# Performance work log

Measured on AMD Instinct MI355X. Metric: run time of the kernel, lower is better.

Reference implementation:

```python
import jax, jax.numpy as jnp
import numpy as np
import math

B, S, D, H = 4, 1024, 1024, 16

def setup_inputs() -> dict:
    key = jax.random.key(0)
    ks = jax.random.split(key, 9)
    Q = jax.random.normal(ks[0], (B, S, D), dtype=jnp.float32)
    K = jax.random.normal(ks[1], (B, S, D), dtype=jnp.float32)
    V = jax.random.normal(ks[2], (B, S, D), dtype=jnp.float32)
    mask = jax.random.randint(ks[3], (B, 1, S, S), 0, 2, dtype=jnp.int32)
    # keep the diagonal unmasked so no causal row is fully -inf (avoids NaN softmax rows)
    eye = jnp.eye(S, dtype=jnp.int32)[None, None]
    mask = jnp.maximum(mask, eye)
    sc = 1.0 / math.sqrt(D)
    Wq = jax.random.normal(ks[4], (D, D), dtype=jnp.float32) * sc
    Wk = jax.random.normal(ks[5], (D, D), dtype=jnp.float32) * sc
    Wv = jax.random.normal(ks[6], (D, D), dtype=jnp.float32) * sc
    Wo = jax.random.normal(ks[7], (D, D), dtype=jnp.float32) * sc
    bo = jnp.zeros((D,), dtype=jnp.float32)
    return {"Q": Q, "K": K, "V": V, "mask": mask,
            "Wq": Wq, "Wk": Wk, "Wv": Wv, "Wo": Wo, "bo": bo, "heads": H}


def reference(Q, K, V, mask, Wq, Wk, Wv, Wo, bo, heads):
    b, s, d = Q.shape
    dk = d // heads
    # QKV projections (bias-free) and head split: [B,S,D] -> [B,H,S,dk]
    def split_heads(x, W):
        return (x @ W).reshape(b, s, heads, dk).transpose(0, 2, 1, 3)
    q = split_heads(Q, Wq)
    k = split_heads(K, Wk)
    v = split_heads(V, Wv)
    # raw scores [B,H,S,S]
    attn = jnp.einsum('bhqd,bhkd->bhqk', q, k) / jnp.sqrt(jnp.float32(dk))
    # multiplicative padding mask
    attn = attn * mask.astype(attn.dtype)
    # sequential=True: torch.tril zeroes the strict upper triangle
    causal = jnp.tril(jnp.ones((s, s), dtype=attn.dtype))
    attn = attn * causal
    # the module's quirk: exact zeros become -inf before softmax
    attn = jnp.where(attn == 0, -jnp.inf, attn)
    scores = jax.nn.softmax(attn, axis=-1)  # dropout is identity in eval / p=0
    ctx = jnp.einsum('bhqk,bhkd->bhqd', scores, v)
    concat = ctx.transpose(0, 2, 1, 3).reshape(b, s, d)
    return concat @ Wo + bo
```

## Files before the change

### kernel.cpp

```cpp
#include <hip/hip_runtime.h>

#define DEV __device__ __forceinline__

typedef __bf16 bf16x8 __attribute__((ext_vector_type(8)));
typedef float f32x4 __attribute__((ext_vector_type(4)));
typedef unsigned short u16x4 __attribute__((ext_vector_type(4)));
typedef unsigned short u16x8 __attribute__((ext_vector_type(8)));
typedef unsigned int u32;

DEV unsigned short f2bf(float f) {
  union { float f; unsigned int u; } v; v.f = f;
  unsigned int r = v.u + 0x7fffu + ((v.u >> 16) & 1u);
  return (unsigned short)(r >> 16);
}

DEV int swz(int row, int kbyte) { return row * 128 + (kbyte ^ ((row & 7) << 4)); }

__global__ __launch_bounds__(256) void pack_mask_k(const int* __restrict__ mask,
                                                   u32* __restrict__ bits) {
  int e = blockIdx.x * 256 + threadIdx.x;
  int m = mask[e];
  unsigned long long b = __ballot(m != 0);
  int lane = threadIdx.x & 63;
  if (lane == 0)       bits[e >> 5] = (u32)b;
  else if (lane == 32) bits[e >> 5] = (u32)(b >> 32);
}

__global__ __launch_bounds__(256) void wtrans_k(
    const float* __restrict__ W0, const float* __restrict__ W1,
    const float* __restrict__ W2, const float* __restrict__ W3,
    unsigned short* __restrict__ O0, unsigned short* __restrict__ O1,
    unsigned short* __restrict__ O2, unsigned short* __restrict__ O3) {
  const float* W = blockIdx.z == 0 ? W0 : blockIdx.z == 1 ? W1 : blockIdx.z == 2 ? W2 : W3;
  unsigned short* O = blockIdx.z == 0 ? O0 : blockIdx.z == 1 ? O1 : blockIdx.z == 2 ? O2 : O3;
  __shared__ float tile[32][33];
  int tx = threadIdx.x, ty = threadIdx.y;
  int x0 = blockIdx.x * 32, y0 = blockIdx.y * 32;
  #pragma unroll
  for (int i = 0; i < 4; i++)
    tile[ty + i * 8][tx] = W[(size_t)(y0 + ty + i * 8) * 1024 + x0 + tx];
  __syncthreads();
  #pragma unroll
  for (int i = 0; i < 4; i++)
    O[(size_t)(x0 + ty + i * 8) * 1024 + y0 + tx] = f2bf(tile[tx][ty + i * 8]);
}

__global__ __launch_bounds__(256) void proj_gemm_k(
    const float* __restrict__ Qx, const float* __restrict__ Kx, const float* __restrict__ Vx,
    const unsigned short* __restrict__ Wtq, const unsigned short* __restrict__ Wtk,
    const unsigned short* __restrict__ Wtv,
    unsigned short* __restrict__ qo, unsigned short* __restrict__ ko,
    unsigned short* __restrict__ vo) {
  int z = blockIdx.z;
  const float* X = z == 0 ? Qx : z == 1 ? Kx : Vx;
  const unsigned short* Wt = z == 0 ? Wtq : z == 1 ? Wtk : Wtv;
  unsigned short* out = z == 0 ? qo : z == 1 ? ko : vo;

  __shared__ __align__(16) unsigned short As[128 * 64];
  __shared__ __align__(16) unsigned short Bs[128 * 64];

  int t = threadIdx.x;
  int m0 = blockIdx.x * 128, n0 = blockIdx.y * 128;
  int w = t >> 6, lane = t & 63;
  int wm = (w >> 1) * 64, wn = (w & 1) * 64;
  int rl = lane & 15, kgrp = lane >> 4;

  f32x4 acc[4][4];
  #pragma unroll
  for (int m = 0; m < 4; m++)
    #pragma unroll
    for (int n = 0; n < 4; n++)
      #pragma unroll
      for (int r = 0; r < 4; r++) acc[m][n][r] = 0.f;

  for (int kt = 0; kt < 16; kt++) {
    __syncthreads();
    #pragma unroll
    for (int i = 0; i < 8; i++) {
      int e = (i * 256 + t) * 4;
      int r = e >> 6, c = e & 63;
      f32x4 xv = *(const f32x4*)(X + (size_t)(m0 + r) * 1024 + kt * 64 + c);
      u16x4 p;
      p[0] = f2bf(xv[0]); p[1] = f2bf(xv[1]); p[2] = f2bf(xv[2]); p[3] = f2bf(xv[3]);
      *(u16x4*)((char*)As + swz(r, c * 2)) = p;
    }
    #pragma unroll
    for (int i = 0; i < 4; i++) {
      int e = (i * 256 + t) * 8;
      int r = e >> 6, c = e & 63;
      u16x8 bv = *(const u16x8*)(Wt + (size_t)(n0 + r) * 1024 + kt * 64 + c);
      *(u16x8*)((char*)Bs + swz(r, c * 2)) = bv;
    }
    __syncthreads();
    #pragma unroll
    for (int kk = 0; kk < 2; kk++) {
      bf16x8 af[4], bfr[4];
      #pragma unroll
      for (int m = 0; m < 4; m++)
        af[m] = *(const bf16x8*)((const char*)As + swz(wm + m * 16 + rl, kk * 64 + kgrp * 16));
      #pragma unroll
      for (int n = 0; n < 4; n++)
        bfr[n] = *(const bf16x8*)((const char*)Bs + swz(wn + n * 16 + rl, kk * 64 + kgrp * 16));
      #pragma unroll
      for (int m = 0; m < 4; m++)
        #pragma unroll
        for (int n = 0; n < 4; n++)
          acc[m][n] = __builtin_amdgcn_mfma_f32_16x16x32_bf16(af[m], bfr[n], acc[m][n], 0, 0, 0);
    }
  }
  #pragma unroll
  for (int m = 0; m < 4; m++)
    #pragma unroll
    for (int n = 0; n < 4; n++)
      #pragma unroll
      for (int r = 0; r < 4; r++) {
        int grow = m0 + wm + m * 16 + kgrp * 4 + r;
        int gcol = n0 + wn + n * 16 + rl;
        int b = grow >> 10, s = grow & 1023;
        int h = gcol >> 6, d = gcol & 63;
        if (z == 2)
          out[(size_t)((b * 16 + h) * 64 + d) * 1024 + s] = f2bf(acc[m][n][r]);
        else
          out[(size_t)((b * 16 + h) * 1024 + s) * 64 + d] = f2bf(acc[m][n][r]);
      }
}

__global__ __launch_bounds__(256) void attn_k(
    const unsigned short* __restrict__ qg, const unsigned short* __restrict__ kg,
    const unsigned short* __restrict__ vtg, const u32* __restrict__ mbits,
    unsigned short* __restrict__ concat) {
  int p = blockIdx.x;
  int bh = blockIdx.y;
  int b = bh >> 4, h = bh & 15;
  int t = threadIdx.x, w = t >> 6, lane = t & 63;
  int rl = lane & 15, kgrp = lane >> 4;

  const int qtA = p, qtB = 15 - p, J = qtB + 1;
  const int q0s[2] = {qtA * 64, qtB * 64};

  __shared__ __align__(16) unsigned short Ks[2][64 * 64];
  __shared__ __align__(16) unsigned short Vt[2][64 * 64];
  __shared__ __align__(16) unsigned short Ps[4][16 * 64];

  const size_t headoff = (size_t)bh * 65536;

  bf16x8 qa[2][2];
  #pragma unroll
  for (int tl = 0; tl < 2; tl++) {
    int row = q0s[tl] + w * 16 + rl;
    #pragma unroll
    for (int kk = 0; kk < 2; kk++)
      qa[tl][kk] = *(const bf16x8*)(qg + headoff + (size_t)row * 64 + kk * 32 + kgrp * 8);
  }

  u16x8 kst[2], vst[2];
  #pragma unroll
  for (int i = 0; i < 2; i++) {
    int e = (i * 256 + t) * 8, r = e >> 6, c = e & 63;
    kst[i] = *(const u16x8*)(kg  + headoff + (size_t)r * 64 + c);
    vst[i] = *(const u16x8*)(vtg + headoff + (size_t)r * 1024 + c);
  }

  float mrow[2][4], lrow[2][4];
  f32x4 acc[2][4];
  #pragma unroll
  for (int tl = 0; tl < 2; tl++)
    #pragma unroll
    for (int r = 0; r < 4; r++) {
      mrow[tl][r] = -1e30f; lrow[tl][r] = 0.f;
      #pragma unroll
      for (int d = 0; d < 4; d++) acc[tl][d][r] = 0.f;
    }

  for (int j = 0; j < J; j++) {
    unsigned short* Kb = (unsigned short*)Ks[j & 1];
    unsigned short* Vb = (unsigned short*)Vt[j & 1];
    #pragma unroll
    for (int i = 0; i < 2; i++) {
      int e = (i * 256 + t) * 8, r = e >> 6, c = e & 63;
      *(u16x8*)((char*)Kb + swz(r, c * 2)) = kst[i];
      *(u16x8*)((char*)Vb + swz(r, c * 2)) = vst[i];
    }
    __syncthreads();
    if (j + 1 < J) {
      #pragma unroll
      for (int i = 0; i < 2; i++) {
        int e = (i * 256 + t) * 8, r = e >> 6, c = e & 63;
        kst[i] = *(const u16x8*)(kg  + headoff + (size_t)((j + 1) * 64 + r) * 64 + c);
        vst[i] = *(const u16x8*)(vtg + headoff + (size_t)r * 1024 + (j + 1) * 64 + c);
      }
    }

    #pragma unroll
    for (int tl = 1; tl >= 0; tl--) {
      if (tl == 0 && j > qtA) continue;
      const int q0 = q0s[tl];
      f32x4 sc[4];
      #pragma unroll
      for (int n = 0; n < 4; n++) {
        f32x4 z4;
        #pragma unroll
        for (int r = 0; r < 4; r++) z4[r] = 0.f;
        bf16x8 kb0 = *(const bf16x8*)((const char*)Kb + swz(n * 16 + rl, 0 * 64 + kgrp * 16));
        bf16x8 kb1 = *(const bf16x8*)((const char*)Kb + swz(n * 16 + rl, 1 * 64 + kgrp * 16));
        z4 = __builtin_amdgcn_mfma_f32_16x16x32_bf16(qa[tl][0], kb0, z4, 0, 0, 0);
        sc[n] = __builtin_amdgcn_mfma_f32_16x16x32_bf16(qa[tl][1], kb1, z4, 0, 0, 0);
      }
      int qrow[4]; u32 w0[4], w1[4];
      #pragma unroll
      for (int r = 0; r < 4; r++) {
        qrow[r] = q0 + w * 16 + kgrp * 4 + r;
        size_t base = ((size_t)b * 1024 + qrow[r]) * 32 + j * 2;
        w0[r] = mbits[base]; w1[r] = mbits[base + 1];
      }
      float pv[4][4];
      #pragma unroll
      for (int n = 0; n < 4; n++) {
        int kvloc = n * 16 + rl;
        int kvg = j * 64 + kvloc;
        #pragma unroll
        for (int r = 0; r < 4; r++) {
          u32 wsel = (n < 2) ? w0[r] : w1[r];
          int bit = (wsel >> (kvloc & 31)) & 1;
          float val = sc[n][r] * 0.125f;
          bool keep = bit && (kvg <= qrow[r]) && (val != 0.f);
          pv[n][r] = keep ? val : -1e30f;
        }
      }
      #pragma unroll
      for (int r = 0; r < 4; r++) {
        float vmax = fmaxf(fmaxf(pv[0][r], pv[1][r]), fmaxf(pv[2][r], pv[3][r]));
        vmax = fmaxf(vmax, __shfl_xor(vmax, 1));
        vmax = fmaxf(vmax, __shfl_xor(vmax, 2));
        vmax = fmaxf(vmax, __shfl_xor(vmax, 4));
        vmax = fmaxf(vmax, __shfl_xor(vmax, 8));
        float mnew = fmaxf(mrow[tl][r], vmax);
        float alpha = __expf(mrow[tl][r] - mnew);
        mrow[tl][r] = mnew;
        float ts = 0.f;
        #pragma unroll
        for (int n = 0; n < 4; n++) {
          float pe = __expf(pv[n][r] - mnew);
          pv[n][r] = pe;
          ts += pe;
        }
        ts += __shfl_xor(ts, 1); ts += __shfl_xor(ts, 2);
        ts += __shfl_xor(ts, 4); ts += __shfl_xor(ts, 8);
        lrow[tl][r] = lrow[tl][r] * alpha + ts;
        #pragma unroll
        for (int d = 0; d < 4; d++) acc[tl][d][r] *= alpha;
      }
      unsigned short* pb = &Ps[w][0];
      #pragma unroll
      for (int n = 0; n < 4; n++) {
        int col = n * 16 + rl;
        #pragma unroll
        for (int r = 0; r < 4; r++)
          *(unsigned short*)((char*)pb + swz(kgrp * 4 + r, col * 2)) = f2bf(pv[n][r]);
      }
      bf16x8 pa[2];
      #pragma unroll
      for (int kk = 0; kk < 2; kk++)
        pa[kk] = *(const bf16x8*)((const char*)pb + swz(rl, kk * 64 + kgrp * 16));
      #pragma unroll
      for (int d = 0; d < 4; d++) {
        bf16x8 vb0 = *(const bf16x8*)((const char*)Vb + swz(d * 16 + rl, 0 * 64 + kgrp * 16));
        bf16x8 vb1 = *(const bf16x8*)((const char*)Vb + swz(d * 16 + rl, 1 * 64 + kgrp * 16));
        acc[tl][d] = __builtin_amdgcn_mfma_f32_16x16x32_bf16(pa[0], vb0, acc[tl][d], 0, 0, 0);
        acc[tl][d] = __builtin_amdgcn_mfma_f32_16x16x32_bf16(pa[1], vb1, acc[tl][d], 0, 0, 0);
      }
    }
  }
  #pragma unroll
  for (int tl = 0; tl < 2; tl++)
    #pragma unroll
    for (int r = 0; r < 4; r++) {
      float linv = 1.f / lrow[tl][r];
      int srow = q0s[tl] + w * 16 + kgrp * 4 + r;
      size_t rowoff = ((size_t)b * 1024 + srow) * 1024 + h * 64;
      #pragma unroll
      for (int d = 0; d < 4; d++)
        concat[rowoff + d * 16 + rl] = f2bf(acc[tl][d][r] * linv);
    }
}

__global__ __launch_bounds__(256) void out_gemm_k(
    const unsigned short* __restrict__ A, const unsigned short* __restrict__ Wt,
    const float* __restrict__ bias, float* __restrict__ out) {
  __shared__ __align__(16) unsigned short As[128 * 64];
  __shared__ __align__(16) unsigned short Bs[128 * 64];

  int t = threadIdx.x;
  int m0 = blockIdx.x * 128, n0 = blockIdx.y * 128;
  int w = t >> 6, lane = t & 63;
  int wm = (w >> 1) * 64, wn = (w & 1) * 64;
  int rl = lane & 15, kgrp = lane >> 4;

  f32x4 acc[4][4];
  #pragma unroll
  for (int m = 0; m < 4; m++)
    #pragma unroll
    for (int n = 0; n < 4; n++)
      #pragma unroll
      for (int r = 0; r < 4; r++) acc[m][n][r] = 0.f;

  for (int kt = 0; kt < 16; kt++) {
    __syncthreads();
    #pragma unroll
    for (int i = 0; i < 4; i++) {
      int e = (i * 256 + t) * 8;
      int r = e >> 6, c = e & 63;
      u16x8 av = *(const u16x8*)(A + (size_t)(m0 + r) * 1024 + kt * 64 + c);
      *(u16x8*)((char*)As + swz(r, c * 2)) = av;
    }
    #pragma unroll
    for (int i = 0; i < 4; i++) {
      int e = (i * 256 + t) * 8;
      int r = e >> 6, c = e & 63;
      u16x8 bv = *(const u16x8*)(Wt + (size_t)(n0 + r) * 1024 + kt * 64 + c);
      *(u16x8*)((char*)Bs + swz(r, c * 2)) = bv;
    }
    __syncthreads();
    #pragma unroll
    for (int kk = 0; kk < 2; kk++) {
      bf16x8 af[4], bfr[4];
      #pragma unroll
      for (int m = 0; m < 4; m++)
        af[m] = *(const bf16x8*)((const char*)As + swz(wm + m * 16 + rl, kk * 64 + kgrp * 16));
      #pragma unroll
      for (int n = 0; n < 4; n++)
        bfr[n] = *(const bf16x8*)((const char*)Bs + swz(wn + n * 16 + rl, kk * 64 + kgrp * 16));
      #pragma unroll
      for (int m = 0; m < 4; m++)
        #pragma unroll
        for (int n = 0; n < 4; n++)
          acc[m][n] = __builtin_amdgcn_mfma_f32_16x16x32_bf16(af[m], bfr[n], acc[m][n], 0, 0, 0);
    }
  }
  #pragma unroll
  for (int m = 0; m < 4; m++)
    #pragma unroll
    for (int n = 0; n < 4; n++)
      #pragma unroll
      for (int r = 0; r < 4; r++) {
        int grow = m0 + wm + m * 16 + kgrp * 4 + r;
        int gcol = n0 + wn + n * 16 + rl;
        out[(size_t)grow * 1024 + gcol] = acc[m][n][r] + bias[gcol];
      }
}

extern "C" void kernel_launch(void* const* d_in, const int* in_sizes, int n_in,
                              void* d_out, int out_size, void* d_ws, size_t ws_size,
                              hipStream_t stream) {
  const float* Q  = (const float*)d_in[0];
  const float* K  = (const float*)d_in[1];
  const float* V  = (const float*)d_in[2];
  const int* mask = (const int*)d_in[3];
  const float* Wq = (const float*)d_in[4];
  const float* Wk = (const float*)d_in[5];
  const float* Wv = (const float*)d_in[6];
  const float* Wo = (const float*)d_in[7];
  const float* bo = (const float*)d_in[8];
  float* out = (float*)d_out;

  char* ws = (char*)d_ws;
  unsigned short* qb  = (unsigned short*)(ws);
  unsigned short* kb  = (unsigned short*)(ws + (8u  << 20));
  unsigned short* vb  = (unsigned short*)(ws + (16u << 20));
  unsigned short* cc  = (unsigned short*)(ws + (24u << 20));
  unsigned short* wqt = (unsigned short*)(ws + (32u << 20));
  unsigned short* wkt = (unsigned short*)(ws + (34u << 20));
  unsigned short* wvt = (unsigned short*)(ws + (36u << 20));
  unsigned short* wot = (unsigned short*)(ws + (38u << 20));
  u32*            mb  = (u32*)(ws + (40u << 20));

  pack_mask_k<<<16384, 256, 0, stream>>>(mask, mb);
  wtrans_k<<<dim3(32, 32, 4), dim3(32, 8), 0, stream>>>(Wq, Wk, Wv, Wo, wqt, wkt, wvt, wot);
  proj_gemm_k<<<dim3(32, 8, 3), 256, 0, stream>>>(Q, K, V, wqt, wkt, wvt, qb, kb, vb);
  attn_k<<<dim3(8, 64), 256, 0, stream>>>(qb, kb, vb, mb, cc);
  out_gemm_k<<<dim3(32, 8), 256, 0, stream>>>(cc, wot, bo, out);
}
```

Baseline: 264.5 us.

## Pre-pack operands into swizzled tiles and load via global_load_lds

Adds a separate kernel that converts Q/K/V to bf16 and stores them pre-tiled in the swizzled LDS layout. The transposed weights, the K/V projection outputs and the attention output are written in the same tile-packed layout. This lets the GEMMs and the attention kernel copy tiles straight from global memory into LDS with global_load_lds, bypassing registers and the per-element swizzle arithmetic. The cost is an extra cast kernel pass over the fp32 inputs and scattered 2-byte stores in the epilogues. The GEMM main loops stay single-buffered.

```diff
diff --git a/kernel.cpp b/kernel.cpp
--- a/kernel.cpp
+++ b/kernel.cpp
@@ -4,7 +4,6 @@
 
 typedef __bf16 bf16x8 __attribute__((ext_vector_type(8)));
 typedef float f32x4 __attribute__((ext_vector_type(4)));
-typedef unsigned short u16x4 __attribute__((ext_vector_type(4)));
 typedef unsigned short u16x8 __attribute__((ext_vector_type(8)));
 typedef unsigned int u32;
 
@@ -15,6 +14,12 @@
 }
 
 DEV int swz(int row, int kbyte) { return row * 128 + (kbyte ^ ((row & 7) << 4)); }
+
+DEV void gload16(const void* g, void* l) {
+  __builtin_amdgcn_global_load_lds(
+      (const __attribute__((address_space(1))) unsigned int*)g,
+      (__attribute__((address_space(3))) unsigned int*)l, 16, 0, 0);
+}
 
 __global__ __launch_bounds__(256) void pack_mask_k(const int* __restrict__ mask,
                                                    u32* __restrict__ bits) {
@@ -24,6 +29,32 @@
   int lane = threadIdx.x & 63;
   if (lane == 0)       bits[e >> 5] = (u32)b;
   else if (lane == 32) bits[e >> 5] = (u32)(b >> 32);
+}
+
+__global__ __launch_bounds__(256) void xcast_k(
+    const float* __restrict__ Qx, const float* __restrict__ Kx, const float* __restrict__ Vx,
+    unsigned short* __restrict__ qp, unsigned short* __restrict__ kp,
+    unsigned short* __restrict__ vp) {
+  int z = blockIdx.y;
+  const float* X = z == 0 ? Qx : z == 1 ? Kx : Vx;
+  unsigned short* P = z == 0 ? qp : z == 1 ? kp : vp;
+  int tile = blockIdx.x;
+  int mb = tile >> 4, kt = tile & 15;
+  int t = threadIdx.x;
+  size_t tb = (size_t)tile * 16384;
+  #pragma unroll
+  for (int i = 0; i < 4; i++) {
+    int idx = i * 256 + t;
+    int r = idx >> 3, j = idx & 7;
+    int c0 = ((j * 16) ^ ((r & 7) << 4)) >> 1;
+    const float* src = X + (size_t)(mb * 128 + r) * 1024 + kt * 64 + c0;
+    f32x4 a = *(const f32x4*)src;
+    f32x4 bq = *(const f32x4*)(src + 4);
+    u16x8 o;
+    o[0] = f2bf(a[0]); o[1] = f2bf(a[1]); o[2] = f2bf(a[2]); o[3] = f2bf(a[3]);
+    o[4] = f2bf(bq[0]); o[5] = f2bf(bq[1]); o[6] = f2bf(bq[2]); o[7] = f2bf(bq[3]);
+    *(u16x8*)((char*)P + tb + (size_t)idx * 16) = o;
+  }
 }
 
 __global__ __launch_bounds__(256) void wtrans_k(
@@ -41,27 +72,29 @@
     tile[ty + i * 8][tx] = W[(size_t)(y0 + ty + i * 8) * 1024 + x0 + tx];
   __syncthreads();
   #pragma unroll
-  for (int i = 0; i < 4; i++)
-    O[(size_t)(x0 + ty + i * 8) * 1024 + y0 + tx] = f2bf(tile[tx][ty + i * 8]);
+  for (int i = 0; i < 4; i++) {
+    int n = x0 + ty + i * 8, k = y0 + tx;
+    size_t a = (size_t)((n >> 7) * 16 + (k >> 6)) * 16384 + swz(n & 127, (k & 63) * 2);
+    *(unsigned short*)((char*)O + a) = f2bf(tile[tx][ty + i * 8]);
+  }
 }
 
 __global__ __launch_bounds__(256) void proj_gemm_k(
-    const float* __restrict__ Qx, const float* __restrict__ Kx, const float* __restrict__ Vx,
+    const unsigned short* __restrict__ Qp, const unsigned short* __restrict__ Kp,
+    const unsigned short* __restrict__ Vp,
     const unsigned short* __restrict__ Wtq, const unsigned short* __restrict__ Wtk,
     const unsigned short* __restrict__ Wtv,
     unsigned short* __restrict__ qo, unsigned short* __restrict__ ko,
     unsigned short* __restrict__ vo) {
   int z = blockIdx.z;
-  const float* X = z == 0 ? Qx : z == 1 ? Kx : Vx;
-  const unsigned short* Wt = z == 0 ? Wtq : z == 1 ? Wtk : Wtv;
+  const unsigned short* Ap = z == 0 ? Qp : z == 1 ? Kp : Vp;
+  const unsigned short* Bp = z == 0 ? Wtq : z == 1 ? Wtk : Wtv;
   unsigned short* out = z == 0 ? qo : z == 1 ? ko : vo;
 
-  __shared__ __align__(16) unsigned short As[128 * 64];
-  __shared__ __align__(16) unsigned short Bs[128 * 64];
-
-  int t = threadIdx.x;
-  int m0 = blockIdx.x * 128, n0 = blockIdx.y * 128;
-  int w = t >> 6, lane = t & 63;
+  __shared__ __align__(16) unsigned short As[8192];
+  __shared__ __align__(16) unsigned short Bs[8192];
+
+  int t = threadIdx.x, w = t >> 6, lane = t & 63;
   int wm = (w >> 1) * 64, wn = (w & 1) * 64;
   int rl = lane & 15, kgrp = lane >> 4;
 
@@ -75,21 +108,14 @@
 
   for (int kt = 0; kt < 16; kt++) {
     __syncthreads();
-    #pragma unroll
-    for (int i = 0; i < 8; i++) {
-      int e = (i * 256 + t) * 4;
-      int r = e >> 6, c = e & 63;
-      f32x4 xv = *(const f32x4*)(X + (size_t)(m0 + r) * 1024 + kt * 64 + c);
-      u16x4 p;
-      p[0] = f2bf(xv[0]); p[1] = f2bf(xv[1]); p[2] = f2bf(xv[2]); p[3] = f2bf(xv[3]);
-      *(u16x4*)((char*)As + swz(r, c * 2)) = p;
-    }
+    const char* ab = (const char*)Ap + (size_t)(blockIdx.x * 16 + kt) * 16384 + w * 1024 + lane * 16;
+    const char* bb = (const char*)Bp + (size_t)(blockIdx.y * 16 + kt) * 16384 + w * 1024 + lane * 16;
+    char* al = (char*)As + w * 1024;
+    char* bl = (char*)Bs + w * 1024;
     #pragma unroll
     for (int i = 0; i < 4; i++) {
-      int e = (i * 256 + t) * 8;
-      int r = e >> 6, c = e & 63;
-      u16x8 bv = *(const u16x8*)(Wt + (size_t)(n0 + r) * 1024 + kt * 64 + c);
-      *(u16x8*)((char*)Bs + swz(r, c * 2)) = bv;
+      gload16(ab + i * 4096, al + i * 4096);
+      gload16(bb + i * 4096, bl + i * 4096);
     }
     __syncthreads();
     #pragma unroll
@@ -108,6 +134,7 @@
           acc[m][n] = __builtin_amdgcn_mfma_f32_16x16x32_bf16(af[m], bfr[n], acc[m][n], 0, 0, 0);
     }
   }
+  int m0 = blockIdx.x * 128, n0 = blockIdx.y * 128;
   #pragma unroll
   for (int m = 0; m < 4; m++)
     #pragma unroll
@@ -118,17 +145,23 @@
         int gcol = n0 + wn + n * 16 + rl;
         int b = grow >> 10, s = grow & 1023;
         int h = gcol >> 6, d = gcol & 63;
-        if (z == 2)
-          out[(size_t)((b * 16 + h) * 64 + d) * 1024 + s] = f2bf(acc[m][n][r]);
-        else
-          out[(size_t)((b * 16 + h) * 1024 + s) * 64 + d] = f2bf(acc[m][n][r]);
+        unsigned short val = f2bf(acc[m][n][r]);
+        if (z == 0) {
+          out[(size_t)((b * 16 + h) * 1024 + s) * 64 + d] = val;
+        } else if (z == 1) {
+          *(unsigned short*)((char*)out +
+            (size_t)((b * 16 + h) * 16 + (s >> 6)) * 8192 + swz(s & 63, d * 2)) = val;
+        } else {
+          *(unsigned short*)((char*)out +
+            (size_t)((b * 16 + h) * 16 + (s >> 6)) * 8192 + swz(d, (s & 63) * 2)) = val;
+        }
       }
 }
 
 __global__ __launch_bounds__(256) void attn_k(
-    const unsigned short* __restrict__ qg, const unsigned short* __restrict__ kg,
-    const unsigned short* __restrict__ vtg, const u32* __restrict__ mbits,
-    unsigned short* __restrict__ concat) {
+    const unsigned short* __restrict__ qg, const unsigned short* __restrict__ kp,
+    const unsigned short* __restrict__ vp, const u32* __restrict__ mbits,
+    unsigned short* __restrict__ ccp) {
   int p = blockIdx.x;
   int bh = blockIdx.y;
   int b = bh >> 4, h = bh & 15;
@@ -138,11 +171,13 @@
   const int qtA = p, qtB = 15 - p, J = qtB + 1;
   const int q0s[2] = {qtA * 64, qtB * 64};
 
-  __shared__ __align__(16) unsigned short Ks[2][64 * 64];
-  __shared__ __align__(16) unsigned short Vt[2][64 * 64];
-  __shared__ __align__(16) unsigned short Ps[4][16 * 64];
-
-  const size_t headoff = (size_t)bh * 65536;
+  __shared__ __align__(16) unsigned short Ks[2][4096];
+  __shared__ __align__(16) unsigned short Vs[2][4096];
+  __shared__ __align__(16) unsigned short Ps[4][1024];
+
+  const size_t qoff = (size_t)bh * 65536;
+  const char* kbase = (const char*)kp + (size_t)bh * 131072;
+  const char* vbase = (const char*)vp + (size_t)bh * 131072;
 
   bf16x8 qa[2][2];
   #pragma unroll
@@ -150,15 +185,16 @@
     int row = q0s[tl] + w * 16 + rl;
     #pragma unroll
     for (int kk = 0; kk < 2; kk++)
-      qa[tl][kk] = *(const bf16x8*)(qg + headoff + (size_t)row * 64 + kk * 32 + kgrp * 8);
-  }
-
-  u16x8 kst[2], vst[2];
-  #pragma unroll
-  for (int i = 0; i < 2; i++) {
-    int e = (i * 256 + t) * 8, r = e >> 6, c = e & 63;
-    kst[i] = *(const u16x8*)(kg  + headoff + (size_t)r * 64 + c);
-    vst[i] = *(const u16x8*)(vtg + headoff + (size_t)r * 1024 + c);
+      qa[tl][kk] = *(const bf16x8*)(qg + qoff + (size_t)row * 64 + kk * 32 + kgrp * 8);
+  }
+
+  {
+    const char* kg = kbase + w * 1024 + lane * 16;
+    const char* vg = vbase + w * 1024 + lane * 16;
+    char* kl = (char*)Ks[0] + w * 1024;
+    char* vl = (char*)Vs[0] + w * 1024;
+    gload16(kg, kl); gload16(kg + 4096, kl + 4096);
+    gload16(vg, vl); gload16(vg + 4096, vl + 4096);
   }
 
   float mrow[2][4], lrow[2][4];
@@ -173,23 +209,18 @@
     }
 
   for (int j = 0; j < J; j++) {
-    unsigned short* Kb = (unsigned short*)Ks[j & 1];
-    unsigned short* Vb = (unsigned short*)Vt[j & 1];
-    #pragma unroll
-    for (int i = 0; i < 2; i++) {
-      int e = (i * 256 + t) * 8, r = e >> 6, c = e & 63;
-      *(u16x8*)((char*)Kb + swz(r, c * 2)) = kst[i];
-      *(u16x8*)((char*)Vb + swz(r, c * 2)) = vst[i];
-    }
     __syncthreads();
     if (j + 1 < J) {
-      #pragma unroll
-      for (int i = 0; i < 2; i++) {
-        int e = (i * 256 + t) * 8, r = e >> 6, c = e & 63;
-        kst[i] = *(const u16x8*)(kg  + headoff + (size_t)((j + 1) * 64 + r) * 64 + c);
-        vst[i] = *(const u16x8*)(vtg + headoff + (size_t)r * 1024 + (j + 1) * 64 + c);
-      }
-    }
+      int nb = (j + 1) & 1;
+      const char* kg = kbase + (size_t)(j + 1) * 8192 + w * 1024 + lane * 16;
+      const char* vg = vbase + (size_t)(j + 1) * 8192 + w * 1024 + lane * 16;
+      char* kl = (char*)Ks[nb] + w * 1024;
+      char* vl = (char*)Vs[nb] + w * 1024;
+      gload16(kg, kl); gload16(kg + 4096, kl + 4096);
+      gload16(vg, vl); gload16(vg + 4096, vl + 4096);
+    }
+    const char* Kb = (const char*)Ks[j & 1];
+    const char* Vb = (const char*)Vs[j & 1];
 
     #pragma unroll
     for (int tl = 1; tl >= 0; tl--) {
@@ -201,8 +232,8 @@
         f32x4 z4;
         #pragma unroll
         for (int r = 0; r < 4; r++) z4[r] = 0.f;
-        bf16x8 kb0 = *(const bf16x8*)((const char*)Kb + swz(n * 16 + rl, 0 * 64 + kgrp * 16));
-        bf16x8 kb1 = *(const bf16x8*)((const char*)Kb + swz(n * 16 + rl, 1 * 64 + kgrp * 16));
+        bf16x8 kb0 = *(const bf16x8*)(Kb + swz(n * 16 + rl, 0 * 64 + kgrp * 16));
+        bf16x8 kb1 = *(const bf16x8*)(Kb + swz(n * 16 + rl, 1 * 64 + kgrp * 16));
         z4 = __builtin_amdgcn_mfma_f32_16x16x32_bf16(qa[tl][0], kb0, z4, 0, 0, 0);
         sc[n] = __builtin_amdgcn_mfma_f32_16x16x32_bf16(qa[tl][1], kb1, z4, 0, 0, 0);
       }
@@ -264,8 +295,8 @@
         pa[kk] = *(const bf16x8*)((const char*)pb + swz(rl, kk * 64 + kgrp * 16));
       #pragma unroll
       for (int d = 0; d < 4; d++) {
-        bf16x8 vb0 = *(const bf16x8*)((const char*)Vb + swz(d * 16 + rl, 0 * 64 + kgrp * 16));
-        bf16x8 vb1 = *(const bf16x8*)((const char*)Vb + swz(d * 16 + rl, 1 * 64 + kgrp * 16));
+        bf16x8 vb0 = *(const bf16x8*)(Vb + swz(d * 16 + rl, 0 * 64 + kgrp * 16));
+        bf16x8 vb1 = *(const bf16x8*)(Vb + swz(d * 16 + rl, 1 * 64 + kgrp * 16));
         acc[tl][d] = __builtin_amdgcn_mfma_f32_16x16x32_bf16(pa[0], vb0, acc[tl][d], 0, 0, 0);
         acc[tl][d] = __builtin_amdgcn_mfma_f32_16x16x32_bf16(pa[1], vb1, acc[tl][d], 0, 0, 0);
       }
@@ -277,22 +308,22 @@
     for (int r = 0; r < 4; r++) {
       float linv = 1.f / lrow[tl][r];
       int srow = q0s[tl] + w * 16 + kgrp * 4 + r;
-      size_t rowoff = ((size_t)b * 1024 + srow) * 1024 + h * 64;
+      int grow = b * 1024 + srow;
+      char* tbase = (char*)ccp + (size_t)((grow >> 7) * 16 + h) * 16384;
+      int rr = grow & 127;
       #pragma unroll
       for (int d = 0; d < 4; d++)
-        concat[rowoff + d * 16 + rl] = f2bf(acc[tl][d][r] * linv);
+        *(unsigned short*)(tbase + swz(rr, (d * 16 + rl) * 2)) = f2bf(acc[tl][d][r] * linv);
     }
 }
 
 __global__ __launch_bounds__(256) void out_gemm_k(
-    const unsigned short* __restrict__ A, const unsigned short* __restrict__ Wt,
+    const unsigned short* __restrict__ Ap, const unsigned short* __restrict__ Bp,
     const float* __restrict__ bias, float* __restrict__ out) {
-  __shared__ __align__(16) unsigned short As[128 * 64];
-  __shared__ __align__(16) unsigned short Bs[128 * 64];
-
-  int t = threadIdx.x;
-  int m0 = blockIdx.x * 128, n0 = blockIdx.y * 128;
-  int w = t >> 6, lane = t & 63;
+  __shared__ __align__(16) unsigned short As[8192];
+  __shared__ __align__(16) unsigned short Bs[8192];
+
+  int t = threadIdx.x, w = t >> 6, lane = t & 63;
   int wm = (w >> 1) * 64, wn = (w & 1) * 64;
   int rl = lane & 15, kgrp = lane >> 4;
 
@@ -306,19 +337,14 @@
 
   for (int kt = 0; kt < 16; kt++) {
     __syncthreads();
+    const char* ab = (const char*)Ap + (size_t)(blockIdx.x * 16 + kt) * 16384 + w * 1024 + lane * 16;
+    const char* bb = (const char*)Bp + (size_t)(blockIdx.y * 16 + kt) * 16384 + w * 1024 + lane * 16;
+    char* al = (char*)As + w * 1024;
+    char* bl = (char*)Bs + w * 1024;
     #pragma unroll
     for (int i = 0; i < 4; i++) {
-      int e = (i * 256 + t) * 8;
-      int r = e >> 6, c = e & 63;
-      u16x8 av = *(const u16x8*)(A + (size_t)(m0 + r) * 1024 + kt * 64 + c);
-      *(u16x8*)((char*)As + swz(r, c * 2)) = av;
-    }
-    #pragma unroll
-    for (int i = 0; i < 4; i++) {
-      int e = (i * 256 + t) * 8;
-      int r = e >> 6, c = e & 63;
-      u16x8 bv = *(const u16x8*)(Wt + (size_t)(n0 + r) * 1024 + kt * 64 + c);
-      *(u16x8*)((char*)Bs + swz(r, c * 2)) = bv;
+      gload16(ab + i * 4096, al + i * 4096);
+      gload16(bb + i * 4096, bl + i * 4096);
     }
     __syncthreads();
     #pragma unroll
@@ -337,6 +363,7 @@
           acc[m][n] = __builtin_amdgcn_mfma_f32_16x16x32_bf16(af[m], bfr[n], acc[m][n], 0, 0, 0);
     }
   }
+  int m0 = blockIdx.x * 128, n0 = blockIdx.y * 128;
   #pragma unroll
   for (int m = 0; m < 4; m++)
     #pragma unroll
@@ -364,19 +391,23 @@
   float* out = (float*)d_out;
 
   char* ws = (char*)d_ws;
-  unsigned short* qb  = (unsigned short*)(ws);
-  unsigned short* kb  = (unsigned short*)(ws + (8u  << 20));
-  unsigned short* vb  = (unsigned short*)(ws + (16u << 20));
-  unsigned short* cc  = (unsigned short*)(ws + (24u << 20));
-  unsigned short* wqt = (unsigned short*)(ws + (32u << 20));
-  unsigned short* wkt = (unsigned short*)(ws + (34u << 20));
-  unsigned short* wvt = (unsigned short*)(ws + (36u << 20));
-  unsigned short* wot = (unsigned short*)(ws + (38u << 20));
-  u32*            mb  = (u32*)(ws + (40u << 20));
+  unsigned short* xq  = (unsigned short*)(ws);
+  unsigned short* xk  = (unsigned short*)(ws + (8u  << 20));
+  unsigned short* xv  = (unsigned short*)(ws + (16u << 20));
+  unsigned short* ccp = (unsigned short*)(ws);
+  unsigned short* qb  = (unsigned short*)(ws + (24u << 20));
+  unsigned short* kpk = (unsigned short*)(ws + (32u << 20));
+  unsigned short* vpk = (unsigned short*)(ws + (40u << 20));
+  unsigned short* wqt = (unsigned short*)(ws + (48u << 20));
+  unsigned short* wkt = (unsigned short*)(ws + (50u << 20));
+  unsigned short* wvt = (unsigned short*)(ws + (52u << 20));
+  unsigned short* wot = (unsigned short*)(ws + (54u << 20));
+  u32*            mb  = (u32*)(ws + (56u << 20));
 
   pack_mask_k<<<16384, 256, 0, stream>>>(mask, mb);
+  xcast_k<<<dim3(512, 3), 256, 0, stream>>>(Q, K, V, xq, xk, xv);
   wtrans_k<<<dim3(32, 32, 4), dim3(32, 8), 0, stream>>>(Wq, Wk, Wv, Wo, wqt, wkt, wvt, wot);
-  proj_gemm_k<<<dim3(32, 8, 3), 256, 0, stream>>>(Q, K, V, wqt, wkt, wvt, qb, kb, vb);
-  attn_k<<<dim3(8, 64), 256, 0, stream>>>(qb, kb, vb, mb, cc);
-  out_gemm_k<<<dim3(32, 8), 256, 0, stream>>>(cc, wot, bo, out);
-}
+  proj_gemm_k<<<dim3(32, 8, 3), 256, 0, stream>>>(xq, xk, xv, wqt, wkt, wvt, qb, kpk, vpk);
+  attn_k<<<dim3(8, 64), 256, 0, stream>>>(qb, kpk, vpk, mb, ccp);
+  out_gemm_k<<<dim3(32, 8), 256, 0, stream>>>(ccp, wot, bo, out);
+}
```

Measured after the change: 252.2 us. -4.7%, faster.
